# Optimization experiments

Measured on AMD Instinct MI355X. Metric: run time of the kernel, lower is better.

Reference implementation:

```python
import jax, jax.numpy as jnp
import numpy as np
import math

B, C, HH, WW = 4, 256, 64, 64
NUM_HEADS = 4
GROUPS = 8
EPS = 1e-5


def setup_inputs() -> dict:
    key = jax.random.key(0)
    k1, k2, k3 = jax.random.split(key, 3)
    x = jax.random.normal(k1, (B, C, HH, WW), dtype=jnp.float32)
    gn_w = jnp.ones((C,), dtype=jnp.float32)
    gn_b = jnp.zeros((C,), dtype=jnp.float32)
    qkv_w = jax.random.normal(k2, (3 * C, C), dtype=jnp.float32) * (1.0 / math.sqrt(C))
    qkv_b = jnp.zeros((3 * C,), dtype=jnp.float32)
    proj_w = jax.random.normal(k3, (C, C), dtype=jnp.float32) * (1.0 / math.sqrt(C))
    proj_b = jnp.zeros((C,), dtype=jnp.float32)
    return {"x": x, "gn_w": gn_w, "gn_b": gn_b, "qkv_w": qkv_w,
            "qkv_b": qkv_b, "proj_w": proj_w, "proj_b": proj_b}


def reference(x, gn_w, gn_b, qkv_w, qkv_b, proj_w, proj_b):
    b, c, h, w = x.shape
    nh = NUM_HEADS
    d = c // nh          # head dim = 64
    s = h * w            # sequence length = 4096

    # GroupNorm(8, c): normalize over (c//G, h, w) per group, biased variance
    xg = x.reshape(b, GROUPS, c // GROUPS, h, w)
    mu = xg.mean(axis=(2, 3, 4), keepdims=True)
    var = xg.var(axis=(2, 3, 4), keepdims=True)
    xn = ((xg - mu) * jax.lax.rsqrt(var + EPS)).reshape(b, c, h, w)
    xn = xn * gn_w[None, :, None, None] + gn_b[None, :, None, None]

    # 1x1 conv QKV == channel-wise matmul
    qkv = jnp.einsum('oc,bchw->bohw', qkv_w, xn) + qkv_b[None, :, None, None]
    qkv = qkv.reshape(b, 3, nh, d, s)
    q = jnp.transpose(qkv[:, 0], (0, 1, 3, 2))  # [b, nh, s, d]
    k = jnp.transpose(qkv[:, 1], (0, 1, 3, 2))
    v = jnp.transpose(qkv[:, 2], (0, 1, 3, 2))

    scale = 1.0 / math.sqrt(d)
    attn = jnp.einsum('bhqd,bhkd->bhqk', q, k) * scale  # [b, nh, s, s]
    attn = jax.nn.softmax(attn, axis=-1)
    out = jnp.einsum('bhqk,bhkd->bhqd', attn, v)        # [b, nh, s, d]

    out = jnp.transpose(out, (0, 1, 3, 2)).reshape(b, c, h, w)
    out = jnp.einsum('oc,bchw->bohw', proj_w, out) + proj_b[None, :, None, None]
    return out + x
```

## Files before the change

### kernel.cpp

```cpp
#include <hip/hip_runtime.h>
#include <hip/hip_bf16.h>

#define B_ 4
#define C_ 256
#define S_ 4096
#define NH_ 4
#define HD_ 64
#define LOG2E 1.4426950408889634f
#define QSC 0.18033688011112042f

typedef __attribute__((ext_vector_type(8))) short short8;
typedef __attribute__((ext_vector_type(4))) short short4v;
typedef __attribute__((ext_vector_type(4))) float f32x4;
typedef __attribute__((ext_vector_type(16))) float f32x16;
typedef __attribute__((ext_vector_type(4))) unsigned uint4v;

static __device__ __forceinline__ short f2bf(float f) {
  unsigned u = __builtin_bit_cast(unsigned, f);
  u += 0x7fffu + ((u >> 16) & 1u);
  return (short)(u >> 16);
}
static __device__ __forceinline__ float bf2f(short h) {
  unsigned u = ((unsigned)(unsigned short)h) << 16;
  return __builtin_bit_cast(float, u);
}

#if __has_builtin(__builtin_amdgcn_exp2f)
#define EXP2(x) __builtin_amdgcn_exp2f(x)
#else
#define EXP2(x) exp2f(x)
#endif

static __device__ __forceinline__ unsigned pkbf(float a, float b) {
  unsigned r;
  asm("v_cvt_pk_bf16_f32 %0, %1, %2" : "=v"(r) : "v"(a), "v"(b));
  return r;
}
static __device__ __forceinline__ void pl32swap(unsigned& a, unsigned& b) {
  asm volatile("v_permlane32_swap_b32 %0, %1" : "+v"(a), "+v"(b));
}
static __device__ __forceinline__ void gl_lds16(const short* g, char* l) {
  __builtin_amdgcn_global_load_lds(
      (const __attribute__((address_space(1))) void*)g,
      (__attribute__((address_space(3))) void*)l, 16, 0, 0);
}

__global__ __launch_bounds__(256) void k_pre(const float* __restrict__ x,
                                             const float* __restrict__ wq,
                                             const float* __restrict__ wp,
                                             float* __restrict__ part,
                                             short* __restrict__ oq,
                                             short* __restrict__ op) {
  int t = threadIdx.x;
  const float* p = x + (size_t)blockIdx.x * 16384;
  float s = 0.f, ss = 0.f;
  const float4* p4 = reinterpret_cast<const float4*>(p);
  for (int i = t; i < 4096; i += 256) {
    float4 v = p4[i];
    s += v.x + v.y + v.z + v.w;
    ss += v.x * v.x + v.y * v.y + v.z * v.z + v.w * v.w;
  }
  for (int m = 1; m < 64; m <<= 1) {
    s += __shfl_xor(s, m, 64);
    ss += __shfl_xor(ss, m, 64);
  }
  __shared__ float rs[4], rss[4];
  int w = t >> 6;
  if ((t & 63) == 0) { rs[w] = s; rss[w] = ss; }
  {
    int i = (blockIdx.x * 256 + t) * 4;
    const int n1 = 768 * 256;
    float sc = 1.f;
    const float* src;
    short* dst;
    if (i < n1) {
      src = wq + i; dst = oq + i;
      if (i < 256 * 256) sc = QSC;
    } else {
      src = wp + (i - n1); dst = op + (i - n1);
    }
    float4 v = *reinterpret_cast<const float4*>(src);
    short4v o;
    o[0] = f2bf(v.x * sc); o[1] = f2bf(v.y * sc);
    o[2] = f2bf(v.z * sc); o[3] = f2bf(v.w * sc);
    *reinterpret_cast<short4v*>(dst) = o;
  }
  __syncthreads();
  if (t == 0) {
    part[2 * blockIdx.x] = rs[0] + rs[1] + rs[2] + rs[3];
    part[2 * blockIdx.x + 1] = rss[0] + rss[1] + rss[2] + rss[3];
  }
}

__global__ __launch_bounds__(256) void k_gn_apply(const float* __restrict__ x,
                                                  const float* __restrict__ gw,
                                                  const float* __restrict__ gb,
                                                  const float* __restrict__ part,
                                                  short* __restrict__ xnt) {
  int st = blockIdx.x;
  int ct = blockIdx.y;
  int b = blockIdx.z;
  int t = threadIdx.x;
  __shared__ short T[64 * 72];
  __shared__ float smu[2], sri[2];
  int c0 = ct * 64, s0 = st * 64;
  if (t < 2) {
    int g = (c0 >> 5) + t;
    int base = b * 64 + g * 8;
    float s = 0.f, ss = 0.f;
    for (int j = 0; j < 8; j++) {
      s += part[2 * (base + j)];
      ss += part[2 * (base + j) + 1];
    }
    float inv = 1.f / (32.f * S_);
    float mu = s * inv;
    float var = ss * inv - mu * mu;
    smu[t] = mu;
    sri[t] = rsqrtf(var + 1e-5f);
  }
  __syncthreads();
  int r4 = t >> 4;
  int f4 = t & 15;
  for (int p = 0; p < 4; p++) {
    int r = p * 16 + r4;
    int c = c0 + r;
    int gl = r >> 5;
    float mu = smu[gl];
    float ri = sri[gl];
    float A = gw[c] * ri;
    float Bb = gb[c] - mu * A;
    float4 v = *reinterpret_cast<const float4*>(x + ((size_t)(b * C_ + c)) * S_ + s0 + f4 * 4);
    int sb = f4 * 4;
    T[(sb + 0) * 72 + r] = f2bf(v.x * A + Bb);
    T[(sb + 1) * 72 + r] = f2bf(v.y * A + Bb);
    T[(sb + 2) * 72 + r] = f2bf(v.z * A + Bb);
    T[(sb + 3) * 72 + r] = f2bf(v.w * A + Bb);
  }
  __syncthreads();
  for (int it = 0; it < 2; it++) {
    int cch = t + it * 256;
    int sl = cch >> 3, c8 = cch & 7;
    short8 v = *reinterpret_cast<short8*>(&T[sl * 72 + c8 * 8]);
    *reinterpret_cast<short8*>(xnt + ((size_t)(b * S_ + s0 + sl)) * C_ + c0 + c8 * 8) = v;
  }
}

template <int MODE, int NSP>
__global__ __launch_bounds__(256) void k_gemm(const short* __restrict__ Wbf,
                                              const short* __restrict__ Xt,
                                              const float* __restrict__ bias,
                                              const float* __restrict__ xres,
                                              short* __restrict__ q_sd,
                                              short* __restrict__ k_sd,
                                              short* __restrict__ v_ds,
                                              long op_stride,
                                              const float* __restrict__ lbufg,
                                              float* __restrict__ outp) {
  int tn = blockIdx.x;
  int tm = blockIdx.y;
  int b = blockIdx.z;
  int t = threadIdx.x;
  __shared__ short lds[4 * 64 * 72];
  char* Al = (char*)lds;
  char* Bl = (char*)lds + 8192;
  short* Blp = lds + 4096;
  int w = t >> 6, lane = t & 63;
  int wr = w >> 1, wc = w & 1;
  int l15 = lane & 15, l4 = lane >> 4;
  int wbg = __builtin_amdgcn_readfirstlane(w) << 10;

  f32x4 acc[4][4];
  for (int m = 0; m < 4; m++)
    for (int n = 0; n < 4; n++)
      for (int j = 0; j < 4; j++) acc[m][n][j] = 0.f;

  const short* Arow = Wbf + (size_t)(tm * 128) * 256;
  const short* Brow = Xt + ((size_t)b * S_ + tn * 128) * 256;

  int r0 = t >> 2, c40 = t & 3;
  int sw0 = (c40 ^ ((r0 >> 1) & 3)) * 8;
  int r1 = (t + 256) >> 2;
  int sw1 = (c40 ^ ((r1 >> 1) & 3)) * 8;

  for (int kk = 0; kk < 256; kk += 32) {
    __syncthreads();
    gl_lds16(Arow + (size_t)r0 * 256 + kk + sw0, Al + wbg);
    gl_lds16(Arow + (size_t)r1 * 256 + kk + sw1, Al + 4096 + wbg);
    if (MODE == 0) {
      gl_lds16(Brow + (size_t)r0 * 256 + kk + sw0, Bl + wbg);
      gl_lds16(Brow + (size_t)r1 * 256 + kk + sw1, Bl + 4096 + wbg);
    } else {
      for (int i = 0; i < 2; i++) {
        int cch = t + i * 256;
        int r = cch >> 2, c4 = cch & 3;
        int c = kk + c4 * 8;
        int bh2 = b * 4 + (c >> 6);
        int d = c & 63;
        int s_glob = tn * 128 + r;
        size_t ro = ((size_t)bh2 * S_ + s_glob) * HD_ + d;
        float a8[8] = {0.f, 0.f, 0.f, 0.f, 0.f, 0.f, 0.f, 0.f};
        float l = 0.f;
#pragma unroll
        for (int i2 = 0; i2 < NSP; i2++) {
          short8 pv = *reinterpret_cast<const short8*>(Xt + (size_t)i2 * op_stride + ro);
#pragma unroll
          for (int j = 0; j < 8; j++) a8[j] += bf2f(pv[j]);
          l += lbufg[(size_t)(i2 * 16 + bh2) * S_ + s_glob];
        }
        float inv = 1.f / l;
        short8 vbv;
#pragma unroll
        for (int j = 0; j < 8; j++) vbv[j] = f2bf(a8[j] * inv);
        *reinterpret_cast<short8*>(&Blp[r * 40 + c4 * 8]) = vbv;
      }
    }
    asm volatile("s_waitcnt vmcnt(0)" ::: "memory");
    __syncthreads();

    short8 af[4], bf[4];
    for (int mt = 0; mt < 4; mt++) {
      int row = wr * 64 + mt * 16 + l15;
      af[mt] = *reinterpret_cast<short8*>(Al + row * 64 + ((l4 ^ ((row >> 1) & 3)) << 4));
    }
    for (int nt = 0; nt < 4; nt++) {
      int row = wc * 64 + nt * 16 + l15;
      if (MODE == 0)
        bf[nt] = *reinterpret_cast<short8*>(Bl + row * 64 + ((l4 ^ ((row >> 1) & 3)) << 4));
      else
        bf[nt] = *reinterpret_cast<short8*>(&Blp[row * 40 + l4 * 8]);
    }
    for (int mt = 0; mt < 4; mt++)
      for (int nt = 0; nt < 4; nt++)
        acc[mt][nt] = __builtin_amdgcn_mfma_f32_16x16x32_bf16(af[mt], bf[nt], acc[mt][nt], 0, 0, 0);
  }
  __syncthreads();

  if (MODE == 0) {
    int o_base = tm * 128 + wr * 64;
    int tt = o_base >> 8;
    int h = (o_base >> 6) & 3;
    int s_base = tn * 128 + wc * 64;
    int bh = b * NH_ + h;
    if (tt == 2) {
      for (int mt = 0; mt < 4; mt++)
        for (int nt = 0; nt < 4; nt++)
          for (int i = 0; i < 4; i++) {
            int o = o_base + mt * 16 + l4 * 4 + i;
            int dd = o & 63;
            int s = s_base + nt * 16 + l15;
            float val = acc[mt][nt][i] + bias[o];
            v_ds[((size_t)bh * HD_ + dd) * S_ + s] = f2bf(val);
          }
    } else {
      float bsc = (tt == 0) ? QSC : 1.f;
      short* T = lds + w * (64 * 72);
      for (int mt = 0; mt < 4; mt++)
        for (int nt = 0; nt < 4; nt++)
          for (int i = 0; i < 4; i++) {
            int o = o_base + mt * 16 + l4 * 4 + i;
            int dd = mt * 16 + l4 * 4 + i;
            int sl = nt * 16 + l15;
            float val = acc[mt][nt][i] + bias[o] * bsc;
            T[sl * 72 + dd] = f2bf(val);
          }
      short* dst = (tt == 0) ? q_sd : k_sd;
      for (int it = 0; it < 8; it++) {
        int cch = lane + it * 64;
        int sl = cch >> 3, c8 = cch & 7;
        short8 v = *reinterpret_cast<short8*>(&T[sl * 72 + c8 * 8]);
        *reinterpret_cast<short8*>(dst + ((size_t)bh * S_ + s_base + sl) * HD_ + c8 * 8) = v;
      }
    }
  } else {
    for (int mt = 0; mt < 4; mt++) {
      int o = tm * 128 + wr * 64 + mt * 16 + l4 * 4;
      for (int nt = 0; nt < 4; nt++) {
        int s = tn * 128 + wc * 64 + nt * 16 + l15;
        for (int i = 0; i < 4; i++) {
          size_t off = ((size_t)(b * C_ + o + i)) * S_ + s;
          outp[off] = acc[mt][nt][i] + bias[o + i] + xres[off];
        }
      }
    }
  }
}

__global__ __launch_bounds__(256, 2) void k_attn(const short* __restrict__ q_sd,
                                                 const short* __restrict__ k_sd,
                                                 const short* __restrict__ v_ds,
                                                 short* __restrict__ op_base,
                                                 long op_stride,
                                                 float* __restrict__ lbuf,
                                                 int ntile) {
  int bid = blockIdx.x;
  int qt = bid >> 5;
  int bh = (bid >> 1) & 15;
  int sk = bid & 1;
  int t = threadIdx.x, w = t >> 6, lane = t & 63;
  int l31 = lane & 31, hi = lane >> 5, hi8 = hi * 8;
  int qb = qt * 256 + w * 64;

  __shared__ char smem[32768];

  int wb = __builtin_amdgcn_readfirstlane(w) << 10;

  int r8 = t >> 3, s8 = t & 7;
  int sw8 = (s8 ^ (r8 & 7)) * 8;
  const short* kb = k_sd + ((size_t)bh * S_ + (size_t)sk * ntile * 64) * HD_;
  const short* vbg = v_ds + (size_t)bh * HD_ * S_ + sk * ntile * 64;
  int koff0 = r8 * 64 + sw8;
  int koff1 = koff0 + 32 * 64;
  size_t voff0 = (size_t)r8 * S_ + sw8;
  size_t voff1 = voff0 + (size_t)32 * S_;

#define STAGE(bsel, ti)                                                        \
  do {                                                                         \
    const short* kt_ = kb + (size_t)(ti) * (64 * HD_);                         \
    const short* vt_ = vbg + (ti) * 64;                                        \
    char* lb_ = smem + ((bsel) << 14) + wb;                                    \
    gl_lds16(kt_ + koff0, lb_);                                                \
    gl_lds16(kt_ + koff1, lb_ + 4096);                                         \
    gl_lds16(vt_ + voff0, lb_ + 8192);                                         \
    gl_lds16(vt_ + voff1, lb_ + 12288);                                        \
  } while (0)

  const short* qpA = q_sd + ((size_t)bh * S_ + qb + l31) * HD_ + hi8;
  short8 qfA[4], qfB[4];
#pragma unroll
  for (int sl = 0; sl < 4; sl++) {
    qfA[sl] = *reinterpret_cast<const short8*>(qpA + sl * 16);
    qfB[sl] = *reinterpret_cast<const short8*>(qpA + 32 * HD_ + sl * 16);
  }

  int x7 = l31 & 7;
  int rb0 = l31 * 128;

  f32x16 OA0, OA1, OB0, OB1;
#pragma unroll
  for (int r = 0; r < 16; r++) { OA0[r] = 0.f; OA1[r] = 0.f; OB0[r] = 0.f; OB1[r] = 0.f; }
  float lA = 0.f, lB = 0.f;

  STAGE(0, 0);
  if (ntile > 1) STAGE(1, 1);
  asm volatile("s_waitcnt vmcnt(0)" ::: "memory");
  __builtin_amdgcn_s_barrier();
  asm volatile("" ::: "memory");

#define MKPA(pa, s0, s1)                                                       \
  do {                                                                         \
    unsigned c0 = pkbf(s0[0], s0[1]), c1 = pkbf(s0[2], s0[3]);                 \
    unsigned c2 = pkbf(s0[4], s0[5]), c3 = pkbf(s0[6], s0[7]);                 \
    pl32swap(c0, c2); pl32swap(c1, c3);                                        \
    uint4v u0; u0[0] = c0; u0[1] = c1; u0[2] = c2; u0[3] = c3;                 \
    pa[0] = __builtin_bit_cast(short8, u0);                                    \
    unsigned c4 = pkbf(s0[8], s0[9]), c5 = pkbf(s0[10], s0[11]);               \
    unsigned c6 = pkbf(s0[12], s0[13]), c7 = pkbf(s0[14], s0[15]);             \
    pl32swap(c4, c6); pl32swap(c5, c7);                                        \
    uint4v u1; u1[0] = c4; u1[1] = c5; u1[2] = c6; u1[3] = c7;                 \
    pa[1] = __builtin_bit_cast(short8, u1);                                    \
    unsigned d0 = pkbf(s1[0], s1[1]), d1 = pkbf(s1[2], s1[3]);                 \
    unsigned d2 = pkbf(s1[4], s1[5]), d3 = pkbf(s1[6], s1[7]);                 \
    pl32swap(d0, d2); pl32swap(d1, d3);                                        \
    uint4v u2; u2[0] = d0; u2[1] = d1; u2[2] = d2; u2[3] = d3;                 \
    pa[2] = __builtin_bit_cast(short8, u2);                                    \
    unsigned d4 = pkbf(s1[8], s1[9]), d5 = pkbf(s1[10], s1[11]);               \
    unsigned d6 = pkbf(s1[12], s1[13]), d7 = pkbf(s1[14], s1[15]);             \
    pl32swap(d4, d6); pl32swap(d5, d7);                                        \
    uint4v u3; u3[0] = d4; u3[1] = d5; u3[2] = d6; u3[3] = d7;                 \
    pa[3] = __builtin_bit_cast(short8, u3);                                    \
  } while (0)

  for (int it = 0; it < ntile; it++) {
    char* cur = smem + ((it & 1) << 14);

    f32x16 sA0, sA1, sB0, sB1;
#pragma unroll
    for (int r = 0; r < 16; r++) { sA0[r] = 0.f; sA1[r] = 0.f; sB0[r] = 0.f; sB1[r] = 0.f; }
    __builtin_amdgcn_s_setprio(1);
#pragma unroll
    for (int sl = 0; sl < 4; sl++) {
      int so = ((sl * 2 + hi) ^ x7) << 4;
      short8 kf0 = *reinterpret_cast<short8*>(cur + rb0 + so);
      short8 kf1 = *reinterpret_cast<short8*>(cur + 4096 + rb0 + so);
      sA0 = __builtin_amdgcn_mfma_f32_32x32x16_bf16(kf0, qfA[sl], sA0, 0, 0, 0);
      sB0 = __builtin_amdgcn_mfma_f32_32x32x16_bf16(kf0, qfB[sl], sB0, 0, 0, 0);
      sA1 = __builtin_amdgcn_mfma_f32_32x32x16_bf16(kf1, qfA[sl], sA1, 0, 0, 0);
      sB1 = __builtin_amdgcn_mfma_f32_32x32x16_bf16(kf1, qfB[sl], sB1, 0, 0, 0);
    }
    __builtin_amdgcn_s_setprio(0);

#pragma unroll
    for (int r = 0; r < 16; r++) sA0[r] = EXP2(sA0[r]);
#pragma unroll
    for (int r = 0; r < 16; r++) sA1[r] = EXP2(sA1[r]);
#pragma unroll
    for (int r = 0; r < 16; r++) sB0[r] = EXP2(sB0[r]);
#pragma unroll
    for (int r = 0; r < 16; r++) sB1[r] = EXP2(sB1[r]);
    {
      float a0 = 0.f, a1 = 0.f, a2 = 0.f, a3 = 0.f;
      float b0 = 0.f, b1 = 0.f, b2 = 0.f, b3 = 0.f;
#pragma unroll
      for (int r = 0; r < 16; r += 4) {
        a0 += sA0[r]; a1 += sA0[r + 1]; a2 += sA0[r + 2]; a3 += sA0[r + 3];
        a0 += sA1[r]; a1 += sA1[r + 1]; a2 += sA1[r + 2]; a3 += sA1[r + 3];
        b0 += sB0[r]; b1 += sB0[r + 1]; b2 += sB0[r + 2]; b3 += sB0[r + 3];
        b0 += sB1[r]; b1 += sB1[r + 1]; b2 += sB1[r + 2]; b3 += sB1[r + 3];
      }
      float rsA = (a0 + a1) + (a2 + a3);
      float rsB = (b0 + b1) + (b2 + b3);
      rsA += __shfl_xor(rsA, 32, 64);
      rsB += __shfl_xor(rsB, 32, 64);
      lA += rsA;
      lB += rsB;
    }

    short8 paA[4], paB[4];
    MKPA(paA, sA0, sA1);
    MKPA(paB, sB0, sB1);

    __builtin_amdgcn_s_setprio(1);
#pragma unroll
    for (int ks = 0; ks < 4; ks++) {
      int so = ((ks * 2 + hi) ^ x7) << 4;
      short8 vf0 = *reinterpret_cast<short8*>(cur + 8192 + rb0 + so);
      short8 vf1 = *reinterpret_cast<short8*>(cur + 12288 + rb0 + so);
      OA0 = __builtin_amdgcn_mfma_f32_32x32x16_bf16(vf0, paA[ks], OA0, 0, 0, 0);
      OB0 = __builtin_amdgcn_mfma_f32_32x32x16_bf16(vf0, paB[ks], OB0, 0, 0, 0);
      OA1 = __builtin_amdgcn_mfma_f32_32x32x16_bf16(vf1, paA[ks], OA1, 0, 0, 0);
      OB1 = __builtin_amdgcn_mfma_f32_32x32x16_bf16(vf1, paB[ks], OB1, 0, 0, 0);
    }
    __builtin_amdgcn_s_setprio(0);

    if (it + 1 < ntile) {
      __builtin_amdgcn_s_barrier();
      if (it + 2 < ntile) {
        STAGE(it & 1, it + 2);
        asm volatile("s_waitcnt vmcnt(4)" ::: "memory");
      } else {
        asm volatile("s_waitcnt vmcnt(0)" ::: "memory");
      }
      __builtin_amdgcn_s_barrier();
      asm volatile("" ::: "memory");
    }
  }

  short* optrA = op_base + (size_t)sk * op_stride + ((size_t)bh * S_ + qb + l31) * HD_;
  short* optrB = optrA + 32 * HD_;
#pragma unroll
  for (int qd = 0; qd < 4; qd++) {
    short4v a0, a1, b0v, b1v;
#pragma unroll
    for (int i = 0; i < 4; i++) {
      a0[i] = f2bf(OA0[qd * 4 + i]);
      a1[i] = f2bf(OA1[qd * 4 + i]);
      b0v[i] = f2bf(OB0[qd * 4 + i]);
      b1v[i] = f2bf(OB1[qd * 4 + i]);
    }
    int d0 = qd * 8 + hi * 4;
    *reinterpret_cast<short4v*>(optrA + d0) = a0;
    *reinterpret_cast<short4v*>(optrA + 32 + d0) = a1;
    *reinterpret_cast<short4v*>(optrB + d0) = b0v;
    *reinterpret_cast<short4v*>(optrB + 32 + d0) = b1v;
  }
  if (hi == 0) {
    lbuf[(size_t)(sk * 16 + bh) * S_ + qb + l31] = lA;
    lbuf[(size_t)(sk * 16 + bh) * S_ + qb + 32 + l31] = lB;
  }
#undef STAGE
#undef MKPA
}

extern "C" void kernel_launch(void* const* d_in, const int* in_sizes, int n_in,
                              void* d_out, int out_size, void* d_ws, size_t ws_size,
                              hipStream_t stream) {
  const float* x      = (const float*)d_in[0];
  const float* gn_w   = (const float*)d_in[1];
  const float* gn_b   = (const float*)d_in[2];
  const float* qkv_w  = (const float*)d_in[3];
  const float* qkv_b  = (const float*)d_in[4];
  const float* proj_w = (const float*)d_in[5];
  const float* proj_b = (const float*)d_in[6];
  char* ws = (char*)d_ws;
  float* part  = (float*)(ws + 2048);
  short* wqkv  = (short*)(ws + 4096);
  short* wproj = (short*)(ws + 397312);
  short* xnt   = (short*)(ws + 528384);
  short* q_sd  = (short*)(ws + 8916992);
  short* k_sd  = (short*)(ws + 17305600);
  short* v_ds  = (short*)(ws + 25694208);
  short* op_base = xnt;
  long op_stride = (42471424 - 528384) / 2;
  float* lbuf  = (float*)(ws + 50860032);
  float* outp  = (float*)d_out;

  k_pre<<<256, 256, 0, stream>>>(x, qkv_w, proj_w, part, wqkv, wproj);
  k_gn_apply<<<dim3(64, 4, 4), 256, 0, stream>>>(x, gn_w, gn_b, part, xnt);
  k_gemm<0, 0><<<dim3(32, 6, 4), 256, 0, stream>>>(wqkv, xnt, qkv_b, nullptr, q_sd, k_sd, v_ds,
                                                   0, nullptr, nullptr);
  k_attn<<<512, 256, 0, stream>>>(q_sd, k_sd, v_ds, op_base, op_stride, lbuf, 32);
  k_gemm<1, 2><<<dim3(32, 2, 4), 256, 0, stream>>>(wproj, op_base, proj_b, x, nullptr, nullptr,
                                                   nullptr, op_stride, lbuf, outp);
}
```

Baseline: 125.8 us.

## Fuse GroupNorm apply into QKV GEMM B-operand load

Removes the separate k_gn_apply kernel. The QKV GEMM now reads fp32 x directly, applies the per-channel GroupNorm scale and shift (computed once per block into shared memory), converts to bf16 and writes the B tile into LDS. This drops one launch and the write-then-read of the normalized bf16 intermediate. In exchange it gives up the async global-to-LDS loads for B, uses strided scalar fp32 loads (stride S per channel), and redoes the normalization for each of the 6 M-tiles.

```diff
diff --git a/kernel.cpp b/kernel.cpp
--- a/kernel.cpp
+++ b/kernel.cpp
@@ -92,61 +92,12 @@
   }
 }
 
-__global__ __launch_bounds__(256) void k_gn_apply(const float* __restrict__ x,
-                                                  const float* __restrict__ gw,
-                                                  const float* __restrict__ gb,
-                                                  const float* __restrict__ part,
-                                                  short* __restrict__ xnt) {
-  int st = blockIdx.x;
-  int ct = blockIdx.y;
-  int b = blockIdx.z;
-  int t = threadIdx.x;
-  __shared__ short T[64 * 72];
-  __shared__ float smu[2], sri[2];
-  int c0 = ct * 64, s0 = st * 64;
-  if (t < 2) {
-    int g = (c0 >> 5) + t;
-    int base = b * 64 + g * 8;
-    float s = 0.f, ss = 0.f;
-    for (int j = 0; j < 8; j++) {
-      s += part[2 * (base + j)];
-      ss += part[2 * (base + j) + 1];
-    }
-    float inv = 1.f / (32.f * S_);
-    float mu = s * inv;
-    float var = ss * inv - mu * mu;
-    smu[t] = mu;
-    sri[t] = rsqrtf(var + 1e-5f);
-  }
-  __syncthreads();
-  int r4 = t >> 4;
-  int f4 = t & 15;
-  for (int p = 0; p < 4; p++) {
-    int r = p * 16 + r4;
-    int c = c0 + r;
-    int gl = r >> 5;
-    float mu = smu[gl];
-    float ri = sri[gl];
-    float A = gw[c] * ri;
-    float Bb = gb[c] - mu * A;
-    float4 v = *reinterpret_cast<const float4*>(x + ((size_t)(b * C_ + c)) * S_ + s0 + f4 * 4);
-    int sb = f4 * 4;
-    T[(sb + 0) * 72 + r] = f2bf(v.x * A + Bb);
-    T[(sb + 1) * 72 + r] = f2bf(v.y * A + Bb);
-    T[(sb + 2) * 72 + r] = f2bf(v.z * A + Bb);
-    T[(sb + 3) * 72 + r] = f2bf(v.w * A + Bb);
-  }
-  __syncthreads();
-  for (int it = 0; it < 2; it++) {
-    int cch = t + it * 256;
-    int sl = cch >> 3, c8 = cch & 7;
-    short8 v = *reinterpret_cast<short8*>(&T[sl * 72 + c8 * 8]);
-    *reinterpret_cast<short8*>(xnt + ((size_t)(b * S_ + s0 + sl)) * C_ + c0 + c8 * 8) = v;
-  }
-}
-
 template <int MODE, int NSP>
 __global__ __launch_bounds__(256) void k_gemm(const short* __restrict__ Wbf,
+                                              const float* __restrict__ xgn,
+                                              const float* __restrict__ gw,
+                                              const float* __restrict__ gb,
+                                              const float* __restrict__ part,
                                               const short* __restrict__ Xt,
                                               const float* __restrict__ bias,
                                               const float* __restrict__ xres,
@@ -161,21 +112,44 @@
   int b = blockIdx.z;
   int t = threadIdx.x;
   __shared__ short lds[4 * 64 * 72];
+  __shared__ float gnA[256], gnB[256];
+  __shared__ float smu[8], sri[8];
   char* Al = (char*)lds;
-  char* Bl = (char*)lds + 8192;
   short* Blp = lds + 4096;
   int w = t >> 6, lane = t & 63;
   int wr = w >> 1, wc = w & 1;
   int l15 = lane & 15, l4 = lane >> 4;
   int wbg = __builtin_amdgcn_readfirstlane(w) << 10;
 
+  if (MODE == 0) {
+    if (t < 8) {
+      int base = b * 64 + t * 8;
+      float s = 0.f, ss = 0.f;
+      for (int j = 0; j < 8; j++) {
+        s += part[2 * (base + j)];
+        ss += part[2 * (base + j) + 1];
+      }
+      float inv = 1.f / (32.f * S_);
+      float mu = s * inv;
+      float var = ss * inv - mu * mu;
+      smu[t] = mu;
+      sri[t] = rsqrtf(var + 1e-5f);
+    }
+    __syncthreads();
+    {
+      float ri = sri[t >> 5], mu = smu[t >> 5];
+      float A = gw[t] * ri;
+      gnA[t] = A;
+      gnB[t] = gb[t] - mu * A;
+    }
+  }
+
   f32x4 acc[4][4];
   for (int m = 0; m < 4; m++)
     for (int n = 0; n < 4; n++)
       for (int j = 0; j < 4; j++) acc[m][n][j] = 0.f;
 
   const short* Arow = Wbf + (size_t)(tm * 128) * 256;
-  const short* Brow = Xt + ((size_t)b * S_ + tn * 128) * 256;
 
   int r0 = t >> 2, c40 = t & 3;
   int sw0 = (c40 ^ ((r0 >> 1) & 3)) * 8;
@@ -186,13 +160,17 @@
     __syncthreads();
     gl_lds16(Arow + (size_t)r0 * 256 + kk + sw0, Al + wbg);
     gl_lds16(Arow + (size_t)r1 * 256 + kk + sw1, Al + 4096 + wbg);
-    if (MODE == 0) {
-      gl_lds16(Brow + (size_t)r0 * 256 + kk + sw0, Bl + wbg);
-      gl_lds16(Brow + (size_t)r1 * 256 + kk + sw1, Bl + 4096 + wbg);
-    } else {
-      for (int i = 0; i < 2; i++) {
-        int cch = t + i * 256;
-        int r = cch >> 2, c4 = cch & 3;
+    for (int i = 0; i < 2; i++) {
+      int cch = t + i * 256;
+      int r = cch >> 2, c4 = cch & 3;
+      short8 vbv;
+      if (MODE == 0) {
+        int cb = kk + c4 * 8;
+        const float* xp = xgn + ((size_t)(b * C_ + cb)) * S_ + tn * 128 + r;
+#pragma unroll
+        for (int j = 0; j < 8; j++)
+          vbv[j] = f2bf(xp[(size_t)j * S_] * gnA[cb + j] + gnB[cb + j]);
+      } else {
         int c = kk + c4 * 8;
         int bh2 = b * 4 + (c >> 6);
         int d = c & 63;
@@ -208,11 +186,10 @@
           l += lbufg[(size_t)(i2 * 16 + bh2) * S_ + s_glob];
         }
         float inv = 1.f / l;
-        short8 vbv;
 #pragma unroll
         for (int j = 0; j < 8; j++) vbv[j] = f2bf(a8[j] * inv);
-        *reinterpret_cast<short8*>(&Blp[r * 40 + c4 * 8]) = vbv;
-      }
+      }
+      *reinterpret_cast<short8*>(&Blp[r * 40 + c4 * 8]) = vbv;
     }
     asm volatile("s_waitcnt vmcnt(0)" ::: "memory");
     __syncthreads();
@@ -224,10 +201,7 @@
     }
     for (int nt = 0; nt < 4; nt++) {
       int row = wc * 64 + nt * 16 + l15;
-      if (MODE == 0)
-        bf[nt] = *reinterpret_cast<short8*>(Bl + row * 64 + ((l4 ^ ((row >> 1) & 3)) << 4));
-      else
-        bf[nt] = *reinterpret_cast<short8*>(&Blp[row * 40 + l4 * 8]);
+      bf[nt] = *reinterpret_cast<short8*>(&Blp[row * 40 + l4 * 8]);
     }
     for (int mt = 0; mt < 4; mt++)
       for (int nt = 0; nt < 4; nt++)
@@ -485,20 +459,20 @@
   float* part  = (float*)(ws + 2048);
   short* wqkv  = (short*)(ws + 4096);
   short* wproj = (short*)(ws + 397312);
-  short* xnt   = (short*)(ws + 528384);
   short* q_sd  = (short*)(ws + 8916992);
   short* k_sd  = (short*)(ws + 17305600);
   short* v_ds  = (short*)(ws + 25694208);
-  short* op_base = xnt;
+  short* op_base = (short*)(ws + 528384);
   long op_stride = (42471424 - 528384) / 2;
   float* lbuf  = (float*)(ws + 50860032);
   float* outp  = (float*)d_out;
 
   k_pre<<<256, 256, 0, stream>>>(x, qkv_w, proj_w, part, wqkv, wproj);
-  k_gn_apply<<<dim3(64, 4, 4), 256, 0, stream>>>(x, gn_w, gn_b, part, xnt);
-  k_gemm<0, 0><<<dim3(32, 6, 4), 256, 0, stream>>>(wqkv, xnt, qkv_b, nullptr, q_sd, k_sd, v_ds,
+  k_gemm<0, 0><<<dim3(32, 6, 4), 256, 0, stream>>>(wqkv, x, gn_w, gn_b, part, nullptr,
+                                                   qkv_b, nullptr, q_sd, k_sd, v_ds,
                                                    0, nullptr, nullptr);
   k_attn<<<512, 256, 0, stream>>>(q_sd, k_sd, v_ds, op_base, op_stride, lbuf, 32);
-  k_gemm<1, 2><<<dim3(32, 2, 4), 256, 0, stream>>>(wproj, op_base, proj_b, x, nullptr, nullptr,
-                                                   nullptr, op_stride, lbuf, outp);
-}
+  k_gemm<1, 2><<<dim3(32, 2, 4), 256, 0, stream>>>(wproj, nullptr, nullptr, nullptr, nullptr,
+                                                   op_base, proj_b, x, nullptr, nullptr, nullptr,
+                                                   op_stride, lbuf, outp);
+}
```

Result: slower. 131.4 us (+4.4%).

## Double-buffer QKV GEMM loads and triple-buffer K/V tiles in attention

Applied to the files above, without the earlier changes.

The MODE 0 GEMM path now prefetches the next k-slice into a second LDS buffer while MFMAs run on the current one, which removes the sync-load-wait serialization each step. The attention kernel goes from two to three LDS stages, so the tile it+2 prefetch is issued at the top of each iteration and overlaps both QK and PV compute. This also drops one barrier per iteration. In exchange, attention LDS grows to 48KB per block, which may limit occupancy under launch_bounds(256,2), and the reworked stage-rotation and waitcnt logic must stay correct.

```diff
diff --git a/kernel.cpp b/kernel.cpp
--- a/kernel.cpp
+++ b/kernel.cpp
@@ -161,8 +161,7 @@
   int b = blockIdx.z;
   int t = threadIdx.x;
   __shared__ short lds[4 * 64 * 72];
-  char* Al = (char*)lds;
-  char* Bl = (char*)lds + 8192;
+  char* glds = (char*)lds;
   short* Blp = lds + 4096;
   int w = t >> 6, lane = t & 63;
   int wr = w >> 1, wc = w & 1;
@@ -182,14 +181,48 @@
   int r1 = (t + 256) >> 2;
   int sw1 = (c40 ^ ((r1 >> 1) & 3)) * 8;
 
-  for (int kk = 0; kk < 256; kk += 32) {
-    __syncthreads();
-    gl_lds16(Arow + (size_t)r0 * 256 + kk + sw0, Al + wbg);
-    gl_lds16(Arow + (size_t)r1 * 256 + kk + sw1, Al + 4096 + wbg);
-    if (MODE == 0) {
-      gl_lds16(Brow + (size_t)r0 * 256 + kk + sw0, Bl + wbg);
-      gl_lds16(Brow + (size_t)r1 * 256 + kk + sw1, Bl + 4096 + wbg);
-    } else {
+  if (MODE == 0) {
+    gl_lds16(Arow + (size_t)r0 * 256 + sw0, glds + wbg);
+    gl_lds16(Arow + (size_t)r1 * 256 + sw1, glds + 4096 + wbg);
+    gl_lds16(Brow + (size_t)r0 * 256 + sw0, glds + 8192 + wbg);
+    gl_lds16(Brow + (size_t)r1 * 256 + sw1, glds + 12288 + wbg);
+    asm volatile("s_waitcnt vmcnt(0)" ::: "memory");
+    __builtin_amdgcn_s_barrier();
+    asm volatile("" ::: "memory");
+    for (int step = 0; step < 8; step++) {
+      char* cb = glds + ((step & 1) << 14);
+      if (step + 1 < 8) {
+        char* nb = glds + (((step + 1) & 1) << 14);
+        int kk = (step + 1) * 32;
+        gl_lds16(Arow + (size_t)r0 * 256 + kk + sw0, nb + wbg);
+        gl_lds16(Arow + (size_t)r1 * 256 + kk + sw1, nb + 4096 + wbg);
+        gl_lds16(Brow + (size_t)r0 * 256 + kk + sw0, nb + 8192 + wbg);
+        gl_lds16(Brow + (size_t)r1 * 256 + kk + sw1, nb + 12288 + wbg);
+      }
+      short8 af[4], bf[4];
+      for (int mt = 0; mt < 4; mt++) {
+        int row = wr * 64 + mt * 16 + l15;
+        af[mt] = *reinterpret_cast<short8*>(cb + row * 64 + ((l4 ^ ((row >> 1) & 3)) << 4));
+      }
+      for (int nt = 0; nt < 4; nt++) {
+        int row = wc * 64 + nt * 16 + l15;
+        bf[nt] = *reinterpret_cast<short8*>(cb + 8192 + row * 64 + ((l4 ^ ((row >> 1) & 3)) << 4));
+      }
+      for (int mt = 0; mt < 4; mt++)
+        for (int nt = 0; nt < 4; nt++)
+          acc[mt][nt] =
+              __builtin_amdgcn_mfma_f32_16x16x32_bf16(af[mt], bf[nt], acc[mt][nt], 0, 0, 0);
+      if (step + 1 < 8) {
+        asm volatile("s_waitcnt vmcnt(0)" ::: "memory");
+        __builtin_amdgcn_s_barrier();
+        asm volatile("" ::: "memory");
+      }
+    }
+  } else {
+    for (int kk = 0; kk < 256; kk += 32) {
+      __syncthreads();
+      gl_lds16(Arow + (size_t)r0 * 256 + kk + sw0, glds + wbg);
+      gl_lds16(Arow + (size_t)r1 * 256 + kk + sw1, glds + 4096 + wbg);
       for (int i = 0; i < 2; i++) {
         int cch = t + i * 256;
         int r = cch >> 2, c4 = cch & 3;
@@ -213,25 +246,23 @@
         for (int j = 0; j < 8; j++) vbv[j] = f2bf(a8[j] * inv);
         *reinterpret_cast<short8*>(&Blp[r * 40 + c4 * 8]) = vbv;
       }
-    }
-    asm volatile("s_waitcnt vmcnt(0)" ::: "memory");
-    __syncthreads();
-
-    short8 af[4], bf[4];
-    for (int mt = 0; mt < 4; mt++) {
-      int row = wr * 64 + mt * 16 + l15;
-      af[mt] = *reinterpret_cast<short8*>(Al + row * 64 + ((l4 ^ ((row >> 1) & 3)) << 4));
-    }
-    for (int nt = 0; nt < 4; nt++) {
-      int row = wc * 64 + nt * 16 + l15;
-      if (MODE == 0)
-        bf[nt] = *reinterpret_cast<short8*>(Bl + row * 64 + ((l4 ^ ((row >> 1) & 3)) << 4));
-      else
+      asm volatile("s_waitcnt vmcnt(0)" ::: "memory");
+      __syncthreads();
+
+      short8 af[4], bf[4];
+      for (int mt = 0; mt < 4; mt++) {
+        int row = wr * 64 + mt * 16 + l15;
+        af[mt] = *reinterpret_cast<short8*>(glds + row * 64 + ((l4 ^ ((row >> 1) & 3)) << 4));
+      }
+      for (int nt = 0; nt < 4; nt++) {
+        int row = wc * 64 + nt * 16 + l15;
         bf[nt] = *reinterpret_cast<short8*>(&Blp[row * 40 + l4 * 8]);
-    }
-    for (int mt = 0; mt < 4; mt++)
-      for (int nt = 0; nt < 4; nt++)
-        acc[mt][nt] = __builtin_amdgcn_mfma_f32_16x16x32_bf16(af[mt], bf[nt], acc[mt][nt], 0, 0, 0);
+      }
+      for (int mt = 0; mt < 4; mt++)
+        for (int nt = 0; nt < 4; nt++)
+          acc[mt][nt] =
+              __builtin_amdgcn_mfma_f32_16x16x32_bf16(af[mt], bf[nt], acc[mt][nt], 0, 0, 0);
+    }
   }
   __syncthreads();
 
@@ -300,7 +331,7 @@
   int l31 = lane & 31, hi = lane >> 5, hi8 = hi * 8;
   int qb = qt * 256 + w * 64;
 
-  __shared__ char smem[32768];
+  __shared__ char smem[49152];
 
   int wb = __builtin_amdgcn_readfirstlane(w) << 10;
 
@@ -342,7 +373,7 @@
 
   STAGE(0, 0);
   if (ntile > 1) STAGE(1, 1);
-  asm volatile("s_waitcnt vmcnt(0)" ::: "memory");
+  asm volatile("s_waitcnt vmcnt(4)" ::: "memory");
   __builtin_amdgcn_s_barrier();
   asm volatile("" ::: "memory");
 
@@ -370,8 +401,12 @@
     pa[3] = __builtin_bit_cast(short8, u3);                                    \
   } while (0)
 
+  int cs = 0;
   for (int it = 0; it < ntile; it++) {
-    char* cur = smem + ((it & 1) << 14);
+    char* cur = smem + (cs << 14);
+    int ns = (cs == 2) ? 0 : cs + 1;
+    int ps = (cs == 0) ? 2 : cs - 1;
+    if (it + 2 < ntile) STAGE(ps, it + 2);
 
     f32x16 sA0, sA1, sB0, sB1;
 #pragma unroll
@@ -433,16 +468,14 @@
     __builtin_amdgcn_s_setprio(0);
 
     if (it + 1 < ntile) {
-      __builtin_amdgcn_s_barrier();
-      if (it + 2 < ntile) {
-        STAGE(it & 1, it + 2);
+      if (it + 2 < ntile)
         asm volatile("s_waitcnt vmcnt(4)" ::: "memory");
-      } else {
+      else
         asm volatile("s_waitcnt vmcnt(0)" ::: "memory");
-      }
       __builtin_amdgcn_s_barrier();
       asm volatile("" ::: "memory");
     }
+    cs = ns;
   }
 
   short* optrA = op_base + (size_t)sk * op_stride + ((size_t)bh * S_ + qb + l31) * HD_;
```

Measured after the change: 125.4 us. About the same (-0.4%).
